# Kernel optimization log

Measured on AMD Instinct MI355X. Metric: run time of the kernel, lower is better.

## Reference

```python
import jax, jax.numpy as jnp
import numpy as np

N_NODES = 50000
N_EDGES = 400000
D_IN = 512
DIM_H = 256
N_GRAPHS = 64
BN_EPS = 1e-5


def _linear_init(key, din, dout):
    kw, kb = jax.random.split(key)
    s = 1.0 / np.sqrt(din)
    W = jax.random.uniform(kw, (din, dout), jnp.float32, -s, s)
    b = jax.random.uniform(kb, (dout,), jnp.float32, -s, s)
    return W, b


def setup_inputs() -> dict:
    key = jax.random.key(0)
    ks = iter(jax.random.split(key, 64))
    inp = {}
    inp["x"] = jax.random.normal(next(ks), (N_NODES, D_IN), jnp.float32)
    inp["edge_index"] = jax.random.randint(next(ks), (2, N_EDGES), 0, N_NODES, jnp.int32)
    inp["batch"] = jnp.sort(jax.random.randint(next(ks), (N_NODES,), 0, N_GRAPHS, jnp.int32))
    dins = [D_IN, DIM_H, DIM_H]
    for l in range(3):
        p = "c%d_" % (l + 1)
        inp[p + "W1"], inp[p + "b1"] = _linear_init(next(ks), dins[l], DIM_H)
        inp[p + "gamma"] = jax.random.uniform(next(ks), (DIM_H,), jnp.float32, 0.5, 1.5)
        inp[p + "beta"] = 0.1 * jax.random.normal(next(ks), (DIM_H,), jnp.float32)
        inp[p + "mean"] = 0.1 * jax.random.normal(next(ks), (DIM_H,), jnp.float32)
        inp[p + "var"] = jax.random.uniform(next(ks), (DIM_H,), jnp.float32, 0.5, 1.5)
        inp[p + "W2"], inp[p + "b2"] = _linear_init(next(ks), DIM_H, DIM_H)
    inp["lin1_W"], inp["lin1_b"] = _linear_init(next(ks), 3 * DIM_H, 64)
    inp["lin2_W"], inp["lin2_b"] = _linear_init(next(ks), 64, 2)
    return inp


def _gin_layer(x, src, dst, W1, b1, gamma, beta, mean, var, W2, b2):
    # GINConv with eps=0: h_i = MLP(x_i + sum_{j->i} x_j); scatter-add over edges
    agg = jax.ops.segment_sum(x[src], dst, num_segments=x.shape[0])
    h = (x + agg) @ W1 + b1
    # eval-mode BatchNorm1d
    h = jax.nn.relu((h - mean) * jax.lax.rsqrt(var + BN_EPS) * gamma + beta)
    return jax.nn.relu(h @ W2 + b2)


def reference(x, edge_index, batch,
              c1_W1, c1_b1, c1_gamma, c1_beta, c1_mean, c1_var, c1_W2, c1_b2,
              c2_W1, c2_b1, c2_gamma, c2_beta, c2_mean, c2_var, c2_W2, c2_b2,
              c3_W1, c3_b1, c3_gamma, c3_beta, c3_mean, c3_var, c3_W2, c3_b2,
              lin1_W, lin1_b, lin2_W, lin2_b):
    src, dst = edge_index[0], edge_index[1]
    h1 = _gin_layer(x, src, dst, c1_W1, c1_b1, c1_gamma, c1_beta, c1_mean, c1_var, c1_W2, c1_b2)
    h2 = _gin_layer(h1, src, dst, c2_W1, c2_b1, c2_gamma, c2_beta, c2_mean, c2_var, c2_W2, c2_b2)
    h3 = _gin_layer(h2, src, dst, c3_W1, c3_b1, c3_gamma, c3_beta, c3_mean, c3_var, c3_W2, c3_b2)
    # global_add_pool per graph
    p1 = jax.ops.segment_sum(h1, batch, num_segments=N_GRAPHS)
    p2 = jax.ops.segment_sum(h2, batch, num_segments=N_GRAPHS)
    p3 = jax.ops.segment_sum(h3, batch, num_segments=N_GRAPHS)
    h = jnp.concatenate([p1, p2, p3], axis=1)
    h = jax.nn.relu(h @ lin1_W + lin1_b)
    # Dropout(p=0.8) is identity in eval mode
    h = h @ lin2_W + lin2_b
    return (h, jax.nn.log_softmax(h, axis=1))
```

## Files before the change

### kernel.cpp

```cpp
#include <hip/hip_runtime.h>
#include <hip/hip_bf16.h>

#define DIV_UP(a,b) (((a)+(b)-1)/(b))

static const int NN  = 50000;
static const int NE  = 400000;
static const int DIN = 512;
static const int DH  = 256;
static const int NG  = 64;
static const int MAXDEG = 64;

typedef unsigned short u16;
typedef unsigned int   u32;
typedef __attribute__((ext_vector_type(8))) short bf16x8;
typedef __attribute__((ext_vector_type(4))) float f32x4;

#define AS1(p) ((const __attribute__((address_space(1))) void*)(p))
#define AS3(p) ((__attribute__((address_space(3))) void*)(p))

__device__ inline u16 f2bf(float f) {
  u32 u = __float_as_uint(f);
  u += 0x7fffu + ((u >> 16) & 1u);
  return (u16)(u >> 16);
}
__device__ inline float bf2f(u16 h) { return __uint_as_float(((u32)h) << 16); }
__device__ inline void unpack2(u32 u, float& lo, float& hi) {
  lo = __uint_as_float(u << 16);
  hi = __uint_as_float(u & 0xffff0000u);
}
__device__ inline u32 pack2(float lo, float hi) {
  return (u32)f2bf(lo) | ((u32)f2bf(hi) << 16);
}

struct SetupArgs {
  const float* Wsrc[6]; u16* Wdst[6];
  const float* bn[15];
  float* scsh;
  int* cnt; float* PL;
};
static const int NB_W = (131072 + 5 * 65536) / 256;
static const int NB_Z = DIV_UP(NN + NG * 768, 256);

__global__ __launch_bounds__(256) void k_setup(SetupArgs a) {
  int b = blockIdx.x;
  if (b < NB_W) {
    int idx = b * 256 + threadIdx.x;
    if (idx < 131072) {
      int n = idx >> 9, k = idx & 511;
      a.Wdst[0][idx] = f2bf(a.Wsrc[0][(size_t)k * 256 + n]);
    } else {
      int r = idx - 131072;
      int s = 1 + (r >> 16);
      int ri = r & 65535;
      int n = ri >> 8, k = ri & 255;
      a.Wdst[s][ri] = f2bf(a.Wsrc[s][(size_t)k * 256 + n]);
    }
  } else if (b < NB_W + 3) {
    int l = b - NB_W, ch = threadIdx.x;
    float sc = rsqrtf(a.bn[l * 5 + 4][ch] + 1e-5f) * a.bn[l * 5 + 1][ch];
    float sh = (a.bn[l * 5 + 0][ch] - a.bn[l * 5 + 3][ch]) * sc + a.bn[l * 5 + 2][ch];
    a.scsh[l * 512 + ch] = sc;
    a.scsh[l * 512 + 256 + ch] = sh;
  } else {
    int i = (b - NB_W - 3) * 256 + threadIdx.x;
    if (i < NN) a.cnt[i] = 0;
    else if (i - NN < NG * 768) a.PL[i - NN] = 0.f;
  }
}

__global__ __launch_bounds__(256) void k_fill2(const int* __restrict__ src,
                                               const int* __restrict__ dst,
                                               int* __restrict__ cnt,
                                               int* __restrict__ adj, int nE) {
  int e = blockIdx.x * 256 + threadIdx.x;
  if (e >= nE) return;
  int d = dst[e];
  int pos = atomicAdd(&cnt[d], 1);
  if (pos < MAXDEG) adj[(size_t)d * MAXDEG + pos] = src[e];
}

__device__ inline void gather_row(const u16* __restrict__ Y, const int* __restrict__ cnt,
                                  const int* __restrict__ adj, int gr, int c,
                                  float& a0, float& a1, float& a2, float& a3,
                                  float& a4, float& a5, float& a6, float& a7) {
  uint4 v = *(const uint4*)(Y + (size_t)gr * DH + c);
  unpack2(v.x,a0,a1); unpack2(v.y,a2,a3); unpack2(v.z,a4,a5); unpack2(v.w,a6,a7);
  int deg = cnt[gr]; if (deg > MAXDEG) deg = MAXDEG;
  const int* row = adj + (size_t)gr * MAXDEG;
  int e = 0;
  for (; e + 8 <= deg; e += 8) {
    uint4 w[8];
#pragma unroll
    for (int u = 0; u < 8; ++u)
      w[u] = *(const uint4*)(Y + (size_t)row[e + u] * DH + c);
#pragma unroll
    for (int u = 0; u < 8; ++u) {
      float b0,b1,b2,b3,b4,b5,b6,b7;
      unpack2(w[u].x,b0,b1); unpack2(w[u].y,b2,b3);
      unpack2(w[u].z,b4,b5); unpack2(w[u].w,b6,b7);
      a0+=b0; a1+=b1; a2+=b2; a3+=b3; a4+=b4; a5+=b5; a6+=b6; a7+=b7;
    }
  }
  for (; e + 4 <= deg; e += 4) {
    uint4 w[4];
#pragma unroll
    for (int u = 0; u < 4; ++u)
      w[u] = *(const uint4*)(Y + (size_t)row[e + u] * DH + c);
#pragma unroll
    for (int u = 0; u < 4; ++u) {
      float b0,b1,b2,b3,b4,b5,b6,b7;
      unpack2(w[u].x,b0,b1); unpack2(w[u].y,b2,b3);
      unpack2(w[u].z,b4,b5); unpack2(w[u].w,b6,b7);
      a0+=b0; a1+=b1; a2+=b2; a3+=b3; a4+=b4; a5+=b5; a6+=b6; a7+=b7;
    }
  }
  for (; e < deg; ++e) {
    uint4 w = *(const uint4*)(Y + (size_t)row[e] * DH + c);
    float b0,b1,b2,b3,b4,b5,b6,b7;
    unpack2(w.x,b0,b1); unpack2(w.y,b2,b3); unpack2(w.z,b4,b5); unpack2(w.w,b6,b7);
    a0+=b0; a1+=b1; a2+=b2; a3+=b3; a4+=b4; a5+=b5; a6+=b6; a7+=b7;
  }
}

template <int K, int F32A>
__global__ __launch_bounds__(512, 4) void k_gemm1(
    const u16* __restrict__ A, const float* __restrict__ A32,
    const u16* __restrict__ BT, u16* __restrict__ out, int M) {
  const int N = 256;
  __shared__ __align__(16) u16 sm[32768];
  u16* Cs = sm;
  const int bm = blockIdx.x * 128;
  const int tid = threadIdx.x;
  const int lane = tid & 63;
  const int wave = tid >> 6;
  const int wm = (wave >> 2) * 64;
  const int wn = (wave & 3) * 64;
  const int l15 = lane & 15;
  const int l4 = lane >> 4;
  const int sw = (lane >> 1) & 3;
  const int srow = lane >> 2;
  const int sslot = (lane & 3) ^ ((lane >> 3) & 3);

  auto STAGE = [&](int buf, int k0) {
    u16* As = sm + buf * 12288;
    u16* Bs = As + 4096;
    {
      int row = wave * 16 + srow;
      int grA = bm + row; if (grA >= M) grA = M - 1;
      if (F32A) {
        const float* s = A32 + (size_t)grA * K + k0 + sslot * 8;
        float4 f0 = *(const float4*)s;
        float4 f1 = *(const float4*)(s + 4);
        uint4 o;
        o.x = pack2(f0.x, f0.y); o.y = pack2(f0.z, f0.w);
        o.z = pack2(f1.x, f1.y); o.w = pack2(f1.z, f1.w);
        *(uint4*)(As + row * 32 + (lane & 3) * 8) = o;
      } else {
        __builtin_amdgcn_global_load_lds(AS1(A + (size_t)grA * K + k0 + sslot * 8),
                                         AS3(As + wave * 512), 16, 0, 0);
      }
    }
#pragma unroll
    for (int i = 0; i < 2; ++i) {
      int q = wave * 2 + i;
      int row = q * 16 + srow;
      __builtin_amdgcn_global_load_lds(AS1(BT + (size_t)row * K + k0 + sslot * 8),
                                       AS3(Bs + q * 512), 16, 0, 0);
    }
  };

  f32x4 acc[4][4] = {};
  const int nt = K >> 5;
  STAGE(0, 0);
  int cur = 0;
  for (int t = 0; t < nt; ++t) {
    __syncthreads();
    if (t + 1 < nt) STAGE(cur ^ 1, (t + 1) << 5);
    u16* As = sm + cur * 12288;
    u16* Bs = As + 4096;
    bf16x8 af[4], bf_[4];
#pragma unroll
    for (int f = 0; f < 4; ++f) {
      af[f]  = *(const bf16x8*)(As + (wm + f * 16 + l15) * 32 + ((l4 ^ sw) << 3));
      bf_[f] = *(const bf16x8*)(Bs + (wn + f * 16 + l15) * 32 + ((l4 ^ sw) << 3));
    }
#pragma unroll
    for (int i = 0; i < 4; ++i)
#pragma unroll
      for (int j = 0; j < 4; ++j)
        acc[i][j] = __builtin_amdgcn_mfma_f32_16x16x32_bf16(af[i], bf_[j], acc[i][j], 0, 0, 0);
    cur ^= 1;
  }

  __syncthreads();
#pragma unroll
  for (int j = 0; j < 4; ++j) {
    int n = wn + j * 16 + l15;
#pragma unroll
    for (int i = 0; i < 4; ++i) {
#pragma unroll
      for (int r = 0; r < 4; ++r) {
        int row = wm + i * 16 + l4 * 4 + r;
        Cs[row * 256 + n] = f2bf(acc[i][j][r]);
      }
    }
  }
  __syncthreads();
  const int ccol = (tid & 31) * 8;
#pragma unroll
  for (int p = 0; p < 8; ++p) {
    int row = p * 16 + (tid >> 5);
    int gm = bm + row;
    if (gm < M)
      *(uint4*)(out + (size_t)gm * N + ccol) = *(const uint4*)(Cs + row * 256 + ccol);
  }
}

template <int STORE>
__global__ __launch_bounds__(512, 4) void k_gin2(
    const u16* __restrict__ Y, const int* __restrict__ cnt,
    const int* __restrict__ adj, const float* __restrict__ scsh,
    const u16* __restrict__ BT, const float* __restrict__ bias,
    u16* __restrict__ out, const int* __restrict__ batch,
    float* __restrict__ PL, int poolOff, int M) {
  __shared__ __align__(16) u16 At[64 * 256];
  __shared__ __align__(16) u16 Bs[2][8192];
  __shared__ int bsh[64];
  const int bm = blockIdx.x * 64;
  const int tid = threadIdx.x;
  const int lane = tid & 63;
  const int wave = tid >> 6;
  const int wm = (wave >> 2) * 32;
  const int wn = (wave & 3) * 64;
  const int l15 = lane & 15;
  const int l4 = lane >> 4;
  const int sw = (lane >> 1) & 3;
  const int a7 = lane & 7;
  const int sslot = (lane & 3) ^ ((lane >> 3) & 3);

  if (tid < 64) bsh[tid] = (bm + tid < M) ? batch[bm + tid] : -1;

  auto STAGE_B = [&](int buf, int k0) {
#pragma unroll
    for (int i = 0; i < 2; ++i) {
      int q = wave * 2 + i;
      int row = q * 16 + (lane >> 2);
      __builtin_amdgcn_global_load_lds(AS1(BT + (size_t)row * 256 + k0 + sslot * 8),
                                       AS3(&Bs[buf][q * 512]), 16, 0, 0);
    }
  };

  STAGE_B(0, 0);

  {
    const int c = (tid & 31) << 3;
    float4 sc0 = *(const float4*)(scsh + c);
    float4 sc1 = *(const float4*)(scsh + c + 4);
    float4 sh0 = *(const float4*)(scsh + 256 + c);
    float4 sh1 = *(const float4*)(scsh + 256 + c + 4);
    const int slot0 = c >> 3;
#pragma unroll 1
    for (int p = 0; p < 4; ++p) {
      int rl = p * 16 + (tid >> 5);
      int gr = bm + rl; if (gr >= M) gr = M - 1;
      float a0,a1,a2,a3,a4,a5,a6,a7v;
      gather_row(Y, cnt, adj, gr, c, a0,a1,a2,a3,a4,a5,a6,a7v);
      a0 = fmaxf(fmaf(a0, sc0.x, sh0.x), 0.f);
      a1 = fmaxf(fmaf(a1, sc0.y, sh0.y), 0.f);
      a2 = fmaxf(fmaf(a2, sc0.z, sh0.z), 0.f);
      a3 = fmaxf(fmaf(a3, sc0.w, sh0.w), 0.f);
      a4 = fmaxf(fmaf(a4, sc1.x, sh1.x), 0.f);
      a5 = fmaxf(fmaf(a5, sc1.y, sh1.y), 0.f);
      a6 = fmaxf(fmaf(a6, sc1.z, sh1.z), 0.f);
      a7v = fmaxf(fmaf(a7v, sc1.w, sh1.w), 0.f);
      uint4 o;
      o.x = pack2(a0,a1); o.y = pack2(a2,a3); o.z = pack2(a4,a5); o.w = pack2(a6,a7v);
      *(uint4*)(At + rl * 256 + ((slot0 ^ (rl & 7)) << 3)) = o;
    }
  }

  f32x4 acc[2][4] = {};
  int cur = 0;
  for (int t = 0; t < 8; ++t) {
    __syncthreads();
    if (t + 1 < 8) STAGE_B(cur ^ 1, (t + 1) << 5);
    bf16x8 af[2], bf_[4];
#pragma unroll
    for (int f = 0; f < 2; ++f) {
      int row = wm + f * 16 + l15;
      af[f] = *(const bf16x8*)(At + row * 256 + ((((t << 2) + l4) ^ a7) << 3));
    }
#pragma unroll
    for (int j = 0; j < 4; ++j) {
      int row = wn + j * 16 + l15;
      bf_[j] = *(const bf16x8*)(&Bs[cur][row * 32 + ((l4 ^ sw) << 3)]);
    }
#pragma unroll
    for (int i = 0; i < 2; ++i)
#pragma unroll
      for (int j = 0; j < 4; ++j)
        acc[i][j] = __builtin_amdgcn_mfma_f32_16x16x32_bf16(af[i], bf_[j], acc[i][j], 0, 0, 0);
    cur ^= 1;
  }

  __syncthreads();
  u16* Cs = At;
#pragma unroll
  for (int j = 0; j < 4; ++j) {
    int n = wn + j * 16 + l15;
    float sh = bias[n];
#pragma unroll
    for (int i = 0; i < 2; ++i) {
#pragma unroll
      for (int r = 0; r < 4; ++r) {
        int row = wm + i * 16 + l4 * 4 + r;
        Cs[row * 256 + n] = f2bf(fmaxf(acc[i][j][r] + sh, 0.f));
      }
    }
  }
  __syncthreads();

  if (STORE) {
    const int ccol = (tid & 31) * 8;
#pragma unroll
    for (int p = 0; p < 4; ++p) {
      int row = p * 16 + (tid >> 5);
      int gm = bm + row;
      if (gm < M)
        *(uint4*)(out + (size_t)gm * DH + ccol) = *(const uint4*)(Cs + row * 256 + ccol);
    }
  }

  {
    int col = tid & 255;
    int half = tid >> 8;
    float accv = 0.f;
    int cg = bsh[half * 32];
    for (int r = 0; r < 32; ++r) {
      int row = half * 32 + r;
      int g = bsh[row];
      if (g != cg) {
        if (cg >= 0) unsafeAtomicAdd(&PL[cg * 768 + poolOff + col], accv);
        accv = 0.f;
        cg = g;
      }
      accv += bf2f(Cs[row * 256 + col]);
    }
    if (cg >= 0) unsafeAtomicAdd(&PL[cg * 768 + poolOff + col], accv);
  }
}

__global__ __launch_bounds__(64) void k_head1(const float* __restrict__ P,
                                              const float* __restrict__ W,
                                              const float* __restrict__ b,
                                              float* __restrict__ Q) {
  __shared__ float pr[768];
  int g = blockIdx.x, t = threadIdx.x;
  for (int i = t; i < 768; i += 64) pr[i] = P[g * 768 + i];
  __syncthreads();
  float acc = b[t];
  for (int k = 0; k < 768; ++k) acc = fmaf(pr[k], W[k * 64 + t], acc);
  Q[g * 64 + t] = fmaxf(acc, 0.f);
}

__global__ __launch_bounds__(64) void k_head2(const float* __restrict__ Q,
                                              const float* __restrict__ W,
                                              const float* __restrict__ b,
                                              float* __restrict__ out) {
  int g = threadIdx.x;
  if (g >= 64) return;
  float h0 = b[0], h1 = b[1];
  for (int k = 0; k < 64; ++k) {
    float q = Q[g * 64 + k];
    h0 = fmaf(q, W[k * 2 + 0], h0);
    h1 = fmaf(q, W[k * 2 + 1], h1);
  }
  out[g * 2 + 0] = h0;
  out[g * 2 + 1] = h1;
  float m = fmaxf(h0, h1);
  float lse = m + logf(expf(h0 - m) + expf(h1 - m));
  out[128 + g * 2 + 0] = h0 - lse;
  out[128 + g * 2 + 1] = h1 - lse;
}

extern "C" void kernel_launch(void* const* d_in, const int* in_sizes, int n_in,
                              void* d_out, int out_size, void* d_ws,
                              size_t ws_size, hipStream_t stream) {
  const float* x = (const float*)d_in[0];
  const int* ei = (const int*)d_in[1];
  const int* batch = (const int*)d_in[2];
  const float* W1[3]; const float* b1[3]; const float* ga[3]; const float* be[3];
  const float* mu[3]; const float* va[3]; const float* W2[3]; const float* b2[3];
  for (int l = 0; l < 3; ++l) {
    int base = 3 + 8 * l;
    W1[l] = (const float*)d_in[base + 0];
    b1[l] = (const float*)d_in[base + 1];
    ga[l] = (const float*)d_in[base + 2];
    be[l] = (const float*)d_in[base + 3];
    mu[l] = (const float*)d_in[base + 4];
    va[l] = (const float*)d_in[base + 5];
    W2[l] = (const float*)d_in[base + 6];
    b2[l] = (const float*)d_in[base + 7];
  }
  const float* l1W = (const float*)d_in[27];
  const float* l1b = (const float*)d_in[28];
  const float* l2W = (const float*)d_in[29];
  const float* l2b = (const float*)d_in[30];
  const int* src = ei;
  const int* dst = ei + NE;
  float* out = (float*)d_out;

  char* w = (char*)d_ws;
  u16* Yb  = (u16*)w; w += (size_t)NN * DH * 2;
  u16* H1b = (u16*)w; w += (size_t)NN * DH * 2;
  u16* H2b = (u16*)w; w += (size_t)NN * DH * 2;
  u16* W1T[3]; u16* W2T[3];
  W1T[0] = (u16*)w; w += (size_t)DIN * DH * 2;
  for (int l = 1; l < 3; ++l) { W1T[l] = (u16*)w; w += (size_t)DH * DH * 2; }
  for (int l = 0; l < 3; ++l) { W2T[l] = (u16*)w; w += (size_t)DH * DH * 2; }
  float* scsh = (float*)w; w += 3 * 512 * 4;
  float* PL = (float*)w; w += NG * 768 * 4;
  float* Q  = (float*)w; w += NG * 64 * 4;
  int* cnt  = (int*)w; w += (size_t)NN * 4;
  int* adj  = (int*)w; w += (size_t)NN * MAXDEG * 4;

  SetupArgs sa;
  sa.Wsrc[0] = W1[0]; sa.Wdst[0] = W1T[0];
  sa.Wsrc[1] = W1[1]; sa.Wdst[1] = W1T[1];
  sa.Wsrc[2] = W1[2]; sa.Wdst[2] = W1T[2];
  for (int l = 0; l < 3; ++l) { sa.Wsrc[3 + l] = W2[l]; sa.Wdst[3 + l] = W2T[l]; }
  for (int l = 0; l < 3; ++l) {
    sa.bn[l * 5 + 0] = b1[l]; sa.bn[l * 5 + 1] = ga[l]; sa.bn[l * 5 + 2] = be[l];
    sa.bn[l * 5 + 3] = mu[l]; sa.bn[l * 5 + 4] = va[l];
  }
  sa.scsh = scsh; sa.cnt = cnt; sa.PL = PL;
  k_setup<<<NB_W + 3 + NB_Z, 256, 0, stream>>>(sa);

  k_fill2<<<DIV_UP(NE, 256), 256, 0, stream>>>(src, dst, cnt, adj, NE);

  const int g1 = DIV_UP(NN, 128);
  const int g2 = DIV_UP(NN, 64);
  const u16* hin[3] = {nullptr, H1b, H2b};
  u16* hout[3] = {H1b, H2b, H1b};

  for (int l = 0; l < 3; ++l) {
    if (l == 0)
      k_gemm1<512, 1><<<g1, 512, 0, stream>>>(nullptr, x, W1T[0], Yb, NN);
    else
      k_gemm1<256, 0><<<g1, 512, 0, stream>>>(hin[l], nullptr, W1T[l], Yb, NN);
    if (l < 2)
      k_gin2<1><<<g2, 512, 0, stream>>>(Yb, cnt, adj, scsh + l * 512, W2T[l],
                                        b2[l], hout[l], batch, PL, 256 * l, NN);
    else
      k_gin2<0><<<g2, 512, 0, stream>>>(Yb, cnt, adj, scsh + l * 512, W2T[l],
                                        b2[l], hout[l], batch, PL, 256 * l, NN);
  }

  k_head1<<<NG, 64, 0, stream>>>(PL, l1W, l1b, Q);
  k_head2<<<1, 64, 0, stream>>>(Q, l2W, l2b, out);
}
```

Baseline: 268.4 us.

## Pad adjacency with sentinel zero row and gather two rows per thread

The setup kernel now fills the whole adjacency table with a sentinel index that points at an extra all-zero row appended to Yb. The aggregation can therefore always read degree rounded up to a multiple of 8 with no remainder loops. Each thread now gathers two rows at once in one loop of 16 loads, to expose more memory-level parallelism. In exchange it adds a full 12.8 MB adjacency memset each call, wasted padded loads, divergence between the two rows' trip counts, and higher register pressure.

After: 443.8 us. +65.4%, slower.

```diff
diff --git a/kernel.cpp b/kernel.cpp
--- a/kernel.cpp
+++ b/kernel.cpp
@@ -37,9 +37,11 @@
   const float* bn[15];
   float* scsh;
   int* cnt; float* PL;
+  int* adj; u16* Yb;
 };
 static const int NB_W = (131072 + 5 * 65536) / 256;
 static const int NB_Z = DIV_UP(NN + NG * 768, 256);
+static const int NB_A = (NN * MAXDEG / 4) / 256;
 
 __global__ __launch_bounds__(256) void k_setup(SetupArgs a) {
   int b = blockIdx.x;
@@ -61,10 +63,14 @@
     float sh = (a.bn[l * 5 + 0][ch] - a.bn[l * 5 + 3][ch]) * sc + a.bn[l * 5 + 2][ch];
     a.scsh[l * 512 + ch] = sc;
     a.scsh[l * 512 + 256 + ch] = sh;
-  } else {
+  } else if (b < NB_W + 3 + NB_Z) {
     int i = (b - NB_W - 3) * 256 + threadIdx.x;
     if (i < NN) a.cnt[i] = 0;
     else if (i - NN < NG * 768) a.PL[i - NN] = 0.f;
+  } else {
+    int idx = (b - NB_W - 3 - NB_Z) * 256 + threadIdx.x;
+    ((uint4*)a.adj)[idx] = make_uint4(NN, NN, NN, NN);
+    if (idx < 32) ((uint4*)(a.Yb + (size_t)NN * DH))[idx] = make_uint4(0, 0, 0, 0);
   }
 }
 
@@ -77,49 +83,6 @@
   int d = dst[e];
   int pos = atomicAdd(&cnt[d], 1);
   if (pos < MAXDEG) adj[(size_t)d * MAXDEG + pos] = src[e];
-}
-
-__device__ inline void gather_row(const u16* __restrict__ Y, const int* __restrict__ cnt,
-                                  const int* __restrict__ adj, int gr, int c,
-                                  float& a0, float& a1, float& a2, float& a3,
-                                  float& a4, float& a5, float& a6, float& a7) {
-  uint4 v = *(const uint4*)(Y + (size_t)gr * DH + c);
-  unpack2(v.x,a0,a1); unpack2(v.y,a2,a3); unpack2(v.z,a4,a5); unpack2(v.w,a6,a7);
-  int deg = cnt[gr]; if (deg > MAXDEG) deg = MAXDEG;
-  const int* row = adj + (size_t)gr * MAXDEG;
-  int e = 0;
-  for (; e + 8 <= deg; e += 8) {
-    uint4 w[8];
-#pragma unroll
-    for (int u = 0; u < 8; ++u)
-      w[u] = *(const uint4*)(Y + (size_t)row[e + u] * DH + c);
-#pragma unroll
-    for (int u = 0; u < 8; ++u) {
-      float b0,b1,b2,b3,b4,b5,b6,b7;
-      unpack2(w[u].x,b0,b1); unpack2(w[u].y,b2,b3);
-      unpack2(w[u].z,b4,b5); unpack2(w[u].w,b6,b7);
-      a0+=b0; a1+=b1; a2+=b2; a3+=b3; a4+=b4; a5+=b5; a6+=b6; a7+=b7;
-    }
-  }
-  for (; e + 4 <= deg; e += 4) {
-    uint4 w[4];
-#pragma unroll
-    for (int u = 0; u < 4; ++u)
-      w[u] = *(const uint4*)(Y + (size_t)row[e + u] * DH + c);
-#pragma unroll
-    for (int u = 0; u < 4; ++u) {
-      float b0,b1,b2,b3,b4,b5,b6,b7;
-      unpack2(w[u].x,b0,b1); unpack2(w[u].y,b2,b3);
-      unpack2(w[u].z,b4,b5); unpack2(w[u].w,b6,b7);
-      a0+=b0; a1+=b1; a2+=b2; a3+=b3; a4+=b4; a5+=b5; a6+=b6; a7+=b7;
-    }
-  }
-  for (; e < deg; ++e) {
-    uint4 w = *(const uint4*)(Y + (size_t)row[e] * DH + c);
-    float b0,b1,b2,b3,b4,b5,b6,b7;
-    unpack2(w.x,b0,b1); unpack2(w.y,b2,b3); unpack2(w.z,b4,b5); unpack2(w.w,b6,b7);
-    a0+=b0; a1+=b1; a2+=b2; a3+=b3; a4+=b4; a5+=b5; a6+=b6; a7+=b7;
-  }
 }
 
 template <int K, int F32A>
@@ -254,17 +217,51 @@
 
   {
     const int c = (tid & 31) << 3;
-    float4 sc0 = *(const float4*)(scsh + c);
-    float4 sc1 = *(const float4*)(scsh + c + 4);
-    float4 sh0 = *(const float4*)(scsh + 256 + c);
-    float4 sh1 = *(const float4*)(scsh + 256 + c + 4);
     const int slot0 = c >> 3;
 #pragma unroll 1
-    for (int p = 0; p < 4; ++p) {
-      int rl = p * 16 + (tid >> 5);
-      int gr = bm + rl; if (gr >= M) gr = M - 1;
+    for (int p = 0; p < 2; ++p) {
+      int rl0 = p * 16 + (tid >> 5);
+      int rl1 = rl0 + 32;
+      int gr0 = bm + rl0; if (gr0 >= M) gr0 = M - 1;
+      int gr1 = bm + rl1; if (gr1 >= M) gr1 = M - 1;
       float a0,a1,a2,a3,a4,a5,a6,a7v;
-      gather_row(Y, cnt, adj, gr, c, a0,a1,a2,a3,a4,a5,a6,a7v);
+      float b0,b1,b2,b3,b4,b5,b6,b7v;
+      uint4 v0 = *(const uint4*)(Y + (size_t)gr0 * DH + c);
+      uint4 v1 = *(const uint4*)(Y + (size_t)gr1 * DH + c);
+      unpack2(v0.x,a0,a1); unpack2(v0.y,a2,a3); unpack2(v0.z,a4,a5); unpack2(v0.w,a6,a7v);
+      unpack2(v1.x,b0,b1); unpack2(v1.y,b2,b3); unpack2(v1.z,b4,b5); unpack2(v1.w,b6,b7v);
+      int d0 = cnt[gr0]; if (d0 > MAXDEG) d0 = MAXDEG; d0 = (d0 + 7) & ~7;
+      int d1 = cnt[gr1]; if (d1 > MAXDEG) d1 = MAXDEG; d1 = (d1 + 7) & ~7;
+      const int* r0p = adj + (size_t)gr0 * MAXDEG;
+      const int* r1p = adj + (size_t)gr1 * MAXDEG;
+      int dm = d0 > d1 ? d0 : d1;
+      for (int e = 0; e < dm; e += 8) {
+        uint4 w0[8], w1[8];
+#pragma unroll
+        for (int u = 0; u < 8; ++u)
+          w0[u] = *(const uint4*)(Y + (size_t)r0p[e + u] * DH + c);
+#pragma unroll
+        for (int u = 0; u < 8; ++u)
+          w1[u] = *(const uint4*)(Y + (size_t)r1p[e + u] * DH + c);
+#pragma unroll
+        for (int u = 0; u < 8; ++u) {
+          float t0,t1,t2,t3,t4,t5,t6,t7;
+          unpack2(w0[u].x,t0,t1); unpack2(w0[u].y,t2,t3);
+          unpack2(w0[u].z,t4,t5); unpack2(w0[u].w,t6,t7);
+          a0+=t0; a1+=t1; a2+=t2; a3+=t3; a4+=t4; a5+=t5; a6+=t6; a7v+=t7;
+        }
+#pragma unroll
+        for (int u = 0; u < 8; ++u) {
+          float t0,t1,t2,t3,t4,t5,t6,t7;
+          unpack2(w1[u].x,t0,t1); unpack2(w1[u].y,t2,t3);
+          unpack2(w1[u].z,t4,t5); unpack2(w1[u].w,t6,t7);
+          b0+=t0; b1+=t1; b2+=t2; b3+=t3; b4+=t4; b5+=t5; b6+=t6; b7v+=t7;
+        }
+      }
+      float4 sc0 = *(const float4*)(scsh + c);
+      float4 sc1 = *(const float4*)(scsh + c + 4);
+      float4 sh0 = *(const float4*)(scsh + 256 + c);
+      float4 sh1 = *(const float4*)(scsh + 256 + c + 4);
       a0 = fmaxf(fmaf(a0, sc0.x, sh0.x), 0.f);
       a1 = fmaxf(fmaf(a1, sc0.y, sh0.y), 0.f);
       a2 = fmaxf(fmaf(a2, sc0.z, sh0.z), 0.f);
@@ -273,9 +270,19 @@
       a5 = fmaxf(fmaf(a5, sc1.y, sh1.y), 0.f);
       a6 = fmaxf(fmaf(a6, sc1.z, sh1.z), 0.f);
       a7v = fmaxf(fmaf(a7v, sc1.w, sh1.w), 0.f);
-      uint4 o;
-      o.x = pack2(a0,a1); o.y = pack2(a2,a3); o.z = pack2(a4,a5); o.w = pack2(a6,a7v);
-      *(uint4*)(At + rl * 256 + ((slot0 ^ (rl & 7)) << 3)) = o;
+      b0 = fmaxf(fmaf(b0, sc0.x, sh0.x), 0.f);
+      b1 = fmaxf(fmaf(b1, sc0.y, sh0.y), 0.f);
+      b2 = fmaxf(fmaf(b2, sc0.z, sh0.z), 0.f);
+      b3 = fmaxf(fmaf(b3, sc0.w, sh0.w), 0.f);
+      b4 = fmaxf(fmaf(b4, sc1.x, sh1.x), 0.f);
+      b5 = fmaxf(fmaf(b5, sc1.y, sh1.y), 0.f);
+      b6 = fmaxf(fmaf(b6, sc1.z, sh1.z), 0.f);
+      b7v = fmaxf(fmaf(b7v, sc1.w, sh1.w), 0.f);
+      uint4 o0, o1;
+      o0.x = pack2(a0,a1); o0.y = pack2(a2,a3); o0.z = pack2(a4,a5); o0.w = pack2(a6,a7v);
+      o1.x = pack2(b0,b1); o1.y = pack2(b2,b3); o1.z = pack2(b4,b5); o1.w = pack2(b6,b7v);
+      *(uint4*)(At + rl0 * 256 + ((slot0 ^ (rl0 & 7)) << 3)) = o0;
+      *(uint4*)(At + rl1 * 256 + ((slot0 ^ (rl1 & 7)) << 3)) = o1;
     }
   }
 
@@ -411,7 +418,7 @@
   float* out = (float*)d_out;
 
   char* w = (char*)d_ws;
-  u16* Yb  = (u16*)w; w += (size_t)NN * DH * 2;
+  u16* Yb  = (u16*)w; w += (size_t)(NN + 1) * DH * 2;
   u16* H1b = (u16*)w; w += (size_t)NN * DH * 2;
   u16* H2b = (u16*)w; w += (size_t)NN * DH * 2;
   u16* W1T[3]; u16* W2T[3];
@@ -433,8 +440,8 @@
     sa.bn[l * 5 + 0] = b1[l]; sa.bn[l * 5 + 1] = ga[l]; sa.bn[l * 5 + 2] = be[l];
     sa.bn[l * 5 + 3] = mu[l]; sa.bn[l * 5 + 4] = va[l];
   }
-  sa.scsh = scsh; sa.cnt = cnt; sa.PL = PL;
-  k_setup<<<NB_W + 3 + NB_Z, 256, 0, stream>>>(sa);
+  sa.scsh = scsh; sa.cnt = cnt; sa.PL = PL; sa.adj = adj; sa.Yb = Yb;
+  k_setup<<<NB_W + 3 + NB_Z + NB_A, 256, 0, stream>>>(sa);
 
   k_fill2<<<DIV_UP(NE, 256), 256, 0, stream>>>(src, dst, cnt, adj, NE);
 
```

## Split gather into standalone kernel and fuse W2 GEMM with next layer's W1 GEMM

Applied to the files above, without the earlier changes.

Moves the neighbour gather plus BN/ReLU out of the GEMM kernel into its own kernel that writes a bf16 activation buffer. A new fused kernel then runs W2 GEMM, bias, ReLU and pooling, and feeds the result straight from LDS into the next layer's W1 GEMM, so the H1/H2 intermediates are never written and reread. This removes one activation round-trip and one GEMM launch per layer, at the cost of a new global write/read of the gathered buffer. It also adds larger LDS use per block, which may lower occupancy.

After: 275.2 us. 1.03x slower.

```diff
diff --git a/kernel.cpp b/kernel.cpp
--- a/kernel.cpp
+++ b/kernel.cpp
@@ -79,14 +79,20 @@
   if (pos < MAXDEG) adj[(size_t)d * MAXDEG + pos] = src[e];
 }
 
-__device__ inline void gather_row(const u16* __restrict__ Y, const int* __restrict__ cnt,
-                                  const int* __restrict__ adj, int gr, int c,
-                                  float& a0, float& a1, float& a2, float& a3,
-                                  float& a4, float& a5, float& a6, float& a7) {
-  uint4 v = *(const uint4*)(Y + (size_t)gr * DH + c);
+__global__ __launch_bounds__(256) void k_gather_bn(const u16* __restrict__ Y,
+                                                   const int* __restrict__ cnt,
+                                                   const int* __restrict__ adj,
+                                                   const float* __restrict__ scsh,
+                                                   u16* __restrict__ A) {
+  int gid = blockIdx.x * 256 + threadIdx.x;
+  int i = gid >> 5;
+  if (i >= NN) return;
+  int c = (gid & 31) << 3;
+  uint4 v = *(const uint4*)(Y + (size_t)i * DH + c);
+  float a0,a1,a2,a3,a4,a5,a6,a7;
   unpack2(v.x,a0,a1); unpack2(v.y,a2,a3); unpack2(v.z,a4,a5); unpack2(v.w,a6,a7);
-  int deg = cnt[gr]; if (deg > MAXDEG) deg = MAXDEG;
-  const int* row = adj + (size_t)gr * MAXDEG;
+  int deg = cnt[i]; if (deg > MAXDEG) deg = MAXDEG;
+  const int* row = adj + (size_t)i * MAXDEG;
   int e = 0;
   for (; e + 8 <= deg; e += 8) {
     uint4 w[8];
@@ -120,13 +126,27 @@
     unpack2(w.x,b0,b1); unpack2(w.y,b2,b3); unpack2(w.z,b4,b5); unpack2(w.w,b6,b7);
     a0+=b0; a1+=b1; a2+=b2; a3+=b3; a4+=b4; a5+=b5; a6+=b6; a7+=b7;
   }
-}
-
-template <int K, int F32A>
-__global__ __launch_bounds__(512, 4) void k_gemm1(
-    const u16* __restrict__ A, const float* __restrict__ A32,
-    const u16* __restrict__ BT, u16* __restrict__ out, int M) {
-  const int N = 256;
+  float4 sc0 = *(const float4*)(scsh + c);
+  float4 sc1 = *(const float4*)(scsh + c + 4);
+  float4 sh0 = *(const float4*)(scsh + 256 + c);
+  float4 sh1 = *(const float4*)(scsh + 256 + c + 4);
+  a0 = fmaxf(fmaf(a0, sc0.x, sh0.x), 0.f);
+  a1 = fmaxf(fmaf(a1, sc0.y, sh0.y), 0.f);
+  a2 = fmaxf(fmaf(a2, sc0.z, sh0.z), 0.f);
+  a3 = fmaxf(fmaf(a3, sc0.w, sh0.w), 0.f);
+  a4 = fmaxf(fmaf(a4, sc1.x, sh1.x), 0.f);
+  a5 = fmaxf(fmaf(a5, sc1.y, sh1.y), 0.f);
+  a6 = fmaxf(fmaf(a6, sc1.z, sh1.z), 0.f);
+  a7 = fmaxf(fmaf(a7, sc1.w, sh1.w), 0.f);
+  uint4 o;
+  o.x = pack2(a0,a1); o.y = pack2(a2,a3); o.z = pack2(a4,a5); o.w = pack2(a6,a7);
+  *(uint4*)(A + (size_t)i * DH + c) = o;
+}
+
+__global__ __launch_bounds__(512, 4) void k_gemm_x(
+    const float* __restrict__ A32, const u16* __restrict__ BT,
+    u16* __restrict__ out, int M) {
+  const int K = 512, N = 256;
   __shared__ __align__(16) u16 sm[32768];
   u16* Cs = sm;
   const int bm = blockIdx.x * 128;
@@ -147,18 +167,13 @@
     {
       int row = wave * 16 + srow;
       int grA = bm + row; if (grA >= M) grA = M - 1;
-      if (F32A) {
-        const float* s = A32 + (size_t)grA * K + k0 + sslot * 8;
-        float4 f0 = *(const float4*)s;
-        float4 f1 = *(const float4*)(s + 4);
-        uint4 o;
-        o.x = pack2(f0.x, f0.y); o.y = pack2(f0.z, f0.w);
-        o.z = pack2(f1.x, f1.y); o.w = pack2(f1.z, f1.w);
-        *(uint4*)(As + row * 32 + (lane & 3) * 8) = o;
-      } else {
-        __builtin_amdgcn_global_load_lds(AS1(A + (size_t)grA * K + k0 + sslot * 8),
-                                         AS3(As + wave * 512), 16, 0, 0);
-      }
+      const float* s = A32 + (size_t)grA * K + k0 + sslot * 8;
+      float4 f0 = *(const float4*)s;
+      float4 f1 = *(const float4*)(s + 4);
+      uint4 o;
+      o.x = pack2(f0.x, f0.y); o.y = pack2(f0.z, f0.w);
+      o.z = pack2(f1.x, f1.y); o.w = pack2(f1.z, f1.w);
+      *(uint4*)(As + row * 32 + (lane & 3) * 8) = o;
     }
 #pragma unroll
     for (int i = 0; i < 2; ++i) {
@@ -216,15 +231,15 @@
   }
 }
 
-template <int STORE>
-__global__ __launch_bounds__(512, 4) void k_gin2(
-    const u16* __restrict__ Y, const int* __restrict__ cnt,
-    const int* __restrict__ adj, const float* __restrict__ scsh,
-    const u16* __restrict__ BT, const float* __restrict__ bias,
-    u16* __restrict__ out, const int* __restrict__ batch,
+template <int HAS2>
+__global__ __launch_bounds__(512, 4) void k_fused(
+    const u16* __restrict__ Ain, const u16* __restrict__ B1T,
+    const float* __restrict__ bias, const u16* __restrict__ B2T,
+    u16* __restrict__ Yout, const int* __restrict__ batch,
     float* __restrict__ PL, int poolOff, int M) {
-  __shared__ __align__(16) u16 At[64 * 256];
-  __shared__ __align__(16) u16 Bs[2][8192];
+  __shared__ __align__(16) u16 BsL[2][8192];
+  __shared__ __align__(16) u16 AsL[2][2048];
+  __shared__ __align__(16) u16 Cs[16384];
   __shared__ int bsh[64];
   const int bm = blockIdx.x * 64;
   const int tid = threadIdx.x;
@@ -236,65 +251,44 @@
   const int l4 = lane >> 4;
   const int sw = (lane >> 1) & 3;
   const int a7 = lane & 7;
+  const int srow = lane >> 2;
   const int sslot = (lane & 3) ^ ((lane >> 3) & 3);
 
   if (tid < 64) bsh[tid] = (bm + tid < M) ? batch[bm + tid] : -1;
 
-  auto STAGE_B = [&](int buf, int k0) {
+  auto STAGE_A = [&](int buf, int k0) {
+    if (wave < 4) {
+      int q = wave;
+      int row = q * 16 + srow;
+      int gr = bm + row; if (gr >= M) gr = M - 1;
+      __builtin_amdgcn_global_load_lds(AS1(Ain + (size_t)gr * 256 + k0 + sslot * 8),
+                                       AS3(&AsL[buf][q * 512]), 16, 0, 0);
+    }
+  };
+  auto STAGE_B = [&](const u16* BT, int buf, int k0) {
 #pragma unroll
     for (int i = 0; i < 2; ++i) {
       int q = wave * 2 + i;
-      int row = q * 16 + (lane >> 2);
+      int row = q * 16 + srow;
       __builtin_amdgcn_global_load_lds(AS1(BT + (size_t)row * 256 + k0 + sslot * 8),
-                                       AS3(&Bs[buf][q * 512]), 16, 0, 0);
+                                       AS3(&BsL[buf][q * 512]), 16, 0, 0);
     }
   };
 
-  STAGE_B(0, 0);
-
-  {
-    const int c = (tid & 31) << 3;
-    float4 sc0 = *(const float4*)(scsh + c);
-    float4 sc1 = *(const float4*)(scsh + c + 4);
-    float4 sh0 = *(const float4*)(scsh + 256 + c);
-    float4 sh1 = *(const float4*)(scsh + 256 + c + 4);
-    const int slot0 = c >> 3;
-#pragma unroll 1
-    for (int p = 0; p < 4; ++p) {
-      int rl = p * 16 + (tid >> 5);
-      int gr = bm + rl; if (gr >= M) gr = M - 1;
-      float a0,a1,a2,a3,a4,a5,a6,a7v;
-      gather_row(Y, cnt, adj, gr, c, a0,a1,a2,a3,a4,a5,a6,a7v);
-      a0 = fmaxf(fmaf(a0, sc0.x, sh0.x), 0.f);
-      a1 = fmaxf(fmaf(a1, sc0.y, sh0.y), 0.f);
-      a2 = fmaxf(fmaf(a2, sc0.z, sh0.z), 0.f);
-      a3 = fmaxf(fmaf(a3, sc0.w, sh0.w), 0.f);
-      a4 = fmaxf(fmaf(a4, sc1.x, sh1.x), 0.f);
-      a5 = fmaxf(fmaf(a5, sc1.y, sh1.y), 0.f);
-      a6 = fmaxf(fmaf(a6, sc1.z, sh1.z), 0.f);
-      a7v = fmaxf(fmaf(a7v, sc1.w, sh1.w), 0.f);
-      uint4 o;
-      o.x = pack2(a0,a1); o.y = pack2(a2,a3); o.z = pack2(a4,a5); o.w = pack2(a6,a7v);
-      *(uint4*)(At + rl * 256 + ((slot0 ^ (rl & 7)) << 3)) = o;
-    }
-  }
-
   f32x4 acc[2][4] = {};
+  STAGE_A(0, 0); STAGE_B(B1T, 0, 0);
   int cur = 0;
   for (int t = 0; t < 8; ++t) {
     __syncthreads();
-    if (t + 1 < 8) STAGE_B(cur ^ 1, (t + 1) << 5);
+    if (t < 7) { STAGE_A(cur ^ 1, (t + 1) << 5); STAGE_B(B1T, cur ^ 1, (t + 1) << 5); }
+    else if (HAS2) STAGE_B(B2T, cur ^ 1, 0);
     bf16x8 af[2], bf_[4];
 #pragma unroll
-    for (int f = 0; f < 2; ++f) {
-      int row = wm + f * 16 + l15;
-      af[f] = *(const bf16x8*)(At + row * 256 + ((((t << 2) + l4) ^ a7) << 3));
-    }
-#pragma unroll
-    for (int j = 0; j < 4; ++j) {
-      int row = wn + j * 16 + l15;
-      bf_[j] = *(const bf16x8*)(&Bs[cur][row * 32 + ((l4 ^ sw) << 3)]);
-    }
+    for (int f = 0; f < 2; ++f)
+      af[f] = *(const bf16x8*)(&AsL[cur][(wm + f * 16 + l15) * 32 + ((l4 ^ sw) << 3)]);
+#pragma unroll
+    for (int j = 0; j < 4; ++j)
+      bf_[j] = *(const bf16x8*)(&BsL[cur][(wn + j * 16 + l15) * 32 + ((l4 ^ sw) << 3)]);
 #pragma unroll
     for (int i = 0; i < 2; ++i)
 #pragma unroll
@@ -304,49 +298,85 @@
   }
 
   __syncthreads();
-  u16* Cs = At;
 #pragma unroll
   for (int j = 0; j < 4; ++j) {
-    int n = wn + j * 16 + l15;
-    float sh = bias[n];
+    int col = wn + j * 16 + l15;
+    float b = bias[col];
 #pragma unroll
     for (int i = 0; i < 2; ++i) {
 #pragma unroll
       for (int r = 0; r < 4; ++r) {
         int row = wm + i * 16 + l4 * 4 + r;
-        Cs[row * 256 + n] = f2bf(fmaxf(acc[i][j][r] + sh, 0.f));
+        float v = fmaxf(acc[i][j][r] + b, 0.f);
+        Cs[row * 256 + ((((col >> 3) ^ (row & 7)) << 3) | (col & 7))] = f2bf(v);
       }
     }
   }
   __syncthreads();
-
-  if (STORE) {
-    const int ccol = (tid & 31) * 8;
-#pragma unroll
-    for (int p = 0; p < 4; ++p) {
-      int row = p * 16 + (tid >> 5);
-      int gm = bm + row;
-      if (gm < M)
-        *(uint4*)(out + (size_t)gm * DH + ccol) = *(const uint4*)(Cs + row * 256 + ccol);
-    }
-  }
 
   {
     int col = tid & 255;
     int half = tid >> 8;
+    int cslot = col >> 3, crem = col & 7;
     float accv = 0.f;
     int cg = bsh[half * 32];
-    for (int r = 0; r < 32; ++r) {
-      int row = half * 32 + r;
+    for (int r0 = 0; r0 < 32; ++r0) {
+      int row = half * 32 + r0;
       int g = bsh[row];
       if (g != cg) {
         if (cg >= 0) unsafeAtomicAdd(&PL[cg * 768 + poolOff + col], accv);
         accv = 0.f;
         cg = g;
       }
-      accv += bf2f(Cs[row * 256 + col]);
+      accv += bf2f(Cs[row * 256 + (((cslot ^ (row & 7)) << 3) | crem)]);
     }
     if (cg >= 0) unsafeAtomicAdd(&PL[cg * 768 + poolOff + col], accv);
+  }
+
+  if (!HAS2) return;
+
+  f32x4 acc2[2][4] = {};
+  for (int t = 0; t < 8; ++t) {
+    __syncthreads();
+    if (t < 7) STAGE_B(B2T, cur ^ 1, (t + 1) << 5);
+    bf16x8 af[2], bf_[4];
+#pragma unroll
+    for (int f = 0; f < 2; ++f) {
+      int row = wm + f * 16 + l15;
+      af[f] = *(const bf16x8*)(Cs + row * 256 + ((((t << 2) + l4) ^ a7) << 3));
+    }
+#pragma unroll
+    for (int j = 0; j < 4; ++j)
+      bf_[j] = *(const bf16x8*)(&BsL[cur][(wn + j * 16 + l15) * 32 + ((l4 ^ sw) << 3)]);
+#pragma unroll
+    for (int i = 0; i < 2; ++i)
+#pragma unroll
+      for (int j = 0; j < 4; ++j)
+        acc2[i][j] = __builtin_amdgcn_mfma_f32_16x16x32_bf16(af[i], bf_[j], acc2[i][j], 0, 0, 0);
+    cur ^= 1;
+  }
+
+  __syncthreads();
+#pragma unroll
+  for (int j = 0; j < 4; ++j) {
+    int n = wn + j * 16 + l15;
+#pragma unroll
+    for (int i = 0; i < 2; ++i) {
+#pragma unroll
+      for (int r = 0; r < 4; ++r) {
+        int row = wm + i * 16 + l4 * 4 + r;
+        Cs[row * 256 + n] = f2bf(acc2[i][j][r]);
+      }
+    }
+  }
+  __syncthreads();
+  const int ccol = (tid & 31) * 8;
+#pragma unroll
+  for (int p = 0; p < 4; ++p) {
+    int row = p * 16 + (tid >> 5);
+    int gm = bm + row;
+    if (gm < M)
+      *(uint4*)(Yout + (size_t)gm * 256 + ccol) = *(const uint4*)(Cs + row * 256 + ccol);
   }
 }
 
@@ -412,8 +442,7 @@
 
   char* w = (char*)d_ws;
   u16* Yb  = (u16*)w; w += (size_t)NN * DH * 2;
-  u16* H1b = (u16*)w; w += (size_t)NN * DH * 2;
-  u16* H2b = (u16*)w; w += (size_t)NN * DH * 2;
+  u16* Ab  = (u16*)w; w += (size_t)NN * DH * 2;
   u16* W1T[3]; u16* W2T[3];
   W1T[0] = (u16*)w; w += (size_t)DIN * DH * 2;
   for (int l = 1; l < 3; ++l) { W1T[l] = (u16*)w; w += (size_t)DH * DH * 2; }
@@ -440,21 +469,15 @@
 
   const int g1 = DIV_UP(NN, 128);
   const int g2 = DIV_UP(NN, 64);
-  const u16* hin[3] = {nullptr, H1b, H2b};
-  u16* hout[3] = {H1b, H2b, H1b};
-
-  for (int l = 0; l < 3; ++l) {
-    if (l == 0)
-      k_gemm1<512, 1><<<g1, 512, 0, stream>>>(nullptr, x, W1T[0], Yb, NN);
-    else
-      k_gemm1<256, 0><<<g1, 512, 0, stream>>>(hin[l], nullptr, W1T[l], Yb, NN);
-    if (l < 2)
-      k_gin2<1><<<g2, 512, 0, stream>>>(Yb, cnt, adj, scsh + l * 512, W2T[l],
-                                        b2[l], hout[l], batch, PL, 256 * l, NN);
-    else
-      k_gin2<0><<<g2, 512, 0, stream>>>(Yb, cnt, adj, scsh + l * 512, W2T[l],
-                                        b2[l], hout[l], batch, PL, 256 * l, NN);
-  }
+  const int gg = DIV_UP(NN * 32, 256);
+
+  k_gemm_x<<<g1, 512, 0, stream>>>(x, W1T[0], Yb, NN);
+  k_gather_bn<<<gg, 256, 0, stream>>>(Yb, cnt, adj, scsh + 0 * 512, Ab);
+  k_fused<1><<<g2, 512, 0, stream>>>(Ab, W2T[0], b2[0], W1T[1], Yb, batch, PL, 0, NN);
+  k_gather_bn<<<gg, 256, 0, stream>>>(Yb, cnt, adj, scsh + 1 * 512, Ab);
+  k_fused<1><<<g2, 512, 0, stream>>>(Ab, W2T[1], b2[1], W1T[2], Yb, batch, PL, 256, NN);
+  k_gather_bn<<<gg, 256, 0, stream>>>(Yb, cnt, adj, scsh + 2 * 512, Ab);
+  k_fused<0><<<g2, 512, 0, stream>>>(Ab, W2T[2], b2[2], nullptr, nullptr, batch, PL, 512, NN);
 
   k_head1<<<NG, 64, 0, stream>>>(PL, l1W, l1b, Q);
   k_head2<<<1, 64, 0, stream>>>(Q, l2W, l2b, out);
```
